# Optimization experiments

Measured on AMD Instinct MI355X. Metric: run time of the kernel, lower is better.

The kernel has to match this reference:

```python
import jax, jax.numpy as jnp
import numpy as np

B, T, C = 4, 2048, 1024
H = 16
HD = C // H  # 64


def setup_inputs() -> dict:
    key = jax.random.key(0)
    ks = jax.random.split(key, 4)
    x = jax.random.normal(ks[0], (B, T, C), dtype=jnp.float32)
    # c_attn: Linear(C, 3C, bias=False)  (qkv_bias=False)
    w_attn = jax.random.normal(ks[1], (C, 3 * C), dtype=jnp.float32) / np.sqrt(C)
    # c_proj: Linear(C, C) with bias (nn.Linear default)
    w_proj = jax.random.normal(ks[2], (C, C), dtype=jnp.float32) / np.sqrt(C)
    b_proj = jax.random.normal(ks[3], (C,), dtype=jnp.float32) * 0.01
    return {"x": x, "w_attn": w_attn, "w_proj": w_proj, "b_proj": b_proj}


def reference(x, w_attn, w_proj, b_proj):
    b, t, c = x.shape
    qkv = x @ w_attn  # [B,T,3C]
    q, k, v = jnp.split(qkv, 3, axis=-1)
    # [B,H,T,HD]
    q = q.reshape(b, t, H, HD).transpose(0, 2, 1, 3)
    k = k.reshape(b, t, H, HD).transpose(0, 2, 1, 3)
    v = v.reshape(b, t, H, HD).transpose(0, 2, 1, 3)
    scale = 1.0 / np.sqrt(HD)
    attn = jnp.einsum('bhqd,bhkd->bhqk', q, k) * scale  # [B,H,T,T]
    causal = jnp.tril(jnp.ones((t, t), dtype=bool))
    attn = jnp.where(causal, attn, -jnp.inf)
    attn = jax.nn.softmax(attn, axis=-1)
    out = jnp.einsum('bhqk,bhkd->bhqd', attn, v)  # [B,H,T,HD]
    out = out.transpose(0, 2, 1, 3).reshape(b, t, c)
    return out @ w_proj + b_proj
```

## Files before the change

### kernel.cpp

```cpp
#include <hip/hip_runtime.h>

#define BB 4
#define TT 2048
#define CC 1024
#define C3 3072
#define HH 16
#define HD 64
#define BT 8192

#define TS 32
#define TSZ (64 * TS)

typedef __bf16 bf16x8 __attribute__((ext_vector_type(8)));
typedef float floatx4 __attribute__((ext_vector_type(4)));
typedef unsigned uintx2 __attribute__((ext_vector_type(2)));
typedef unsigned short u16;

__device__ __forceinline__ u16 f2bf(float f) {
  union { float f; unsigned u; } a; a.f = f;
  return (u16)((a.u + 0x7fffu + ((a.u >> 16) & 1u)) >> 16);
}
__device__ __forceinline__ bf16x8 ld8(const u16* p) { return *(const bf16x8*)p; }
__device__ __forceinline__ floatx4 mfma16(bf16x8 a, bf16x8 b, floatx4 c) {
  return __builtin_amdgcn_mfma_f32_16x16x32_bf16(a, b, c, 0, 0, 0);
}

__device__ __forceinline__ void qd_xchg(unsigned a, unsigned b,
                                        unsigned& r0, unsigned& r1) {
  uintx2 t = __builtin_amdgcn_permlane32_swap(a, b, false, false);
  uintx2 r = __builtin_amdgcn_permlane16_swap(t[0], t[1], false, false);
  r0 = r[0]; r1 = r[1];
}

__global__ __launch_bounds__(256) void tobf16_kernel(const float4* __restrict__ src,
                                                     ushort4* __restrict__ dst, int n4) {
  int i = blockIdx.x * 256 + threadIdx.x;
  if (i >= n4) return;
  float4 v = src[i];
  ushort4 o; o.x = f2bf(v.x); o.y = f2bf(v.y); o.z = f2bf(v.z); o.w = f2bf(v.w);
  dst[i] = o;
}

__global__ __launch_bounds__(256) void transpose_bf16_kernel(const float* __restrict__ src,
                                                             u16* __restrict__ dst,
                                                             int K, int N) {
  __shared__ float s[64][65];
  const int t = threadIdx.x;
  const int r = t >> 4;
  const int c = (t & 15) * 4;
  const int k0 = blockIdx.y * 64, n0 = blockIdx.x * 64;
#pragma unroll
  for (int i = 0; i < 4; ++i) {
    float4 v = *(const float4*)&src[(size_t)(k0 + r + i * 16) * N + n0 + c];
    s[r + i * 16][c + 0] = v.x; s[r + i * 16][c + 1] = v.y;
    s[r + i * 16][c + 2] = v.z; s[r + i * 16][c + 3] = v.w;
  }
  __syncthreads();
#pragma unroll
  for (int i = 0; i < 4; ++i) {
    const int nn = r + i * 16;
    ushort4 o;
    o.x = f2bf(s[c + 0][nn]); o.y = f2bf(s[c + 1][nn]);
    o.z = f2bf(s[c + 2][nn]); o.w = f2bf(s[c + 3][nn]);
    *(ushort4*)&dst[(size_t)(n0 + nn) * K + k0 + c] = o;
  }
}

template<int MODE>
__global__ __launch_bounds__(256) void gemm_kernel(
    const u16* __restrict__ A, const u16* __restrict__ B,
    const float* __restrict__ bias, float* __restrict__ outf,
    u16* __restrict__ qk, u16* __restrict__ vT,
    int M, int N, int K) {
  __shared__ u16 smem[2][2][2 * TSZ];

  const int t = threadIdx.x;
  const int w = t >> 6, lane = t & 63, lr = lane & 15, qd = lane >> 4;
  const int wm = w >> 1, wn = w & 1;
  const int m0 = blockIdx.y * 128, n0 = blockIdx.x * 128;

  const int sr = t >> 2;
  const int sc = (t & 3) * 8;
  const int so = sr * TS + sc;
  const u16* Ag = A + (size_t)(m0 + sr) * K + sc;
  const u16* Bg = B + (size_t)(n0 + sr) * K + sc;

  floatx4 acc[4][4] = {};

  uint4 rA0, rA1, rB0, rB1;
  rA0 = *(const uint4*)(Ag);
  rA1 = *(const uint4*)(Ag + (size_t)64 * K);
  rB0 = *(const uint4*)(Bg);
  rB1 = *(const uint4*)(Bg + (size_t)64 * K);

  for (int k0 = 0; k0 < K; k0 += 32) {
    const int p = (k0 >> 5) & 1;
    u16* sA = &smem[p][0][0];
    u16* sB = &smem[p][1][0];
    *(uint4*)&sA[so]       = rA0;
    *(uint4*)&sA[TSZ + so] = rA1;
    *(uint4*)&sB[so]       = rB0;
    *(uint4*)&sB[TSZ + so] = rB1;
    __syncthreads();
    if (k0 + 32 < K) {
      rA0 = *(const uint4*)(Ag + k0 + 32);
      rA1 = *(const uint4*)(Ag + (size_t)64 * K + k0 + 32);
      rB0 = *(const uint4*)(Bg + k0 + 32);
      rB1 = *(const uint4*)(Bg + (size_t)64 * K + k0 + 32);
    }

    bf16x8 af[4], bf[4];
#pragma unroll
    for (int mj = 0; mj < 4; ++mj) af[mj] = ld8(&sA[(wm * 64 + mj * 16 + lr) * TS + qd * 8]);
#pragma unroll
    for (int nj = 0; nj < 4; ++nj) bf[nj] = ld8(&sB[(wn * 64 + nj * 16 + lr) * TS + qd * 8]);
#pragma unroll
    for (int mj = 0; mj < 4; ++mj)
#pragma unroll
      for (int nj = 0; nj < 4; ++nj)
        acc[mj][nj] = mfma16(af[mj], bf[nj], acc[mj][nj]);
  }

  const int rowg0 = m0 + wm * 64;
  const int colg0 = n0 + wn * 64;
  if constexpr (MODE == 2) {
#pragma unroll
    for (int nj = 0; nj < 4; ++nj) {
      const int col = colg0 + nj * 16 + lr;
      const float bv = bias[col];
#pragma unroll
      for (int mj = 0; mj < 4; ++mj)
#pragma unroll
        for (int i = 0; i < 4; ++i)
          outf[(size_t)(rowg0 + mj * 16 + qd * 4 + i) * N + col] = acc[mj][nj][i] + bv;
    }
  } else {
    __syncthreads();
    u16* Tw = &smem[0][0][0] + w * (32 * 72);
    const bool isV = (n0 >= 2 * CC);
    if (!isV) {
      const float qs = (n0 < CC) ? 0.18033688011f : 1.0f;
#pragma unroll
      for (int half = 0; half < 2; ++half) {
#pragma unroll
        for (int m2 = 0; m2 < 2; ++m2)
#pragma unroll
          for (int nj = 0; nj < 4; ++nj)
#pragma unroll
            for (int i = 0; i < 4; ++i)
              Tw[(m2 * 16 + qd * 4 + i) * 72 + nj * 16 + lr] =
                  f2bf(acc[half * 2 + m2][nj][i] * qs);
#pragma unroll
        for (int s = 0; s < 4; ++s) {
          const int rl = s * 8 + (lane >> 3);
          const int c0 = (lane & 7) * 8;
          *(bf16x8*)&qk[(size_t)(rowg0 + half * 32 + rl) * (2 * CC) + colg0 + c0] =
              ld8(&Tw[rl * 72 + c0]);
        }
      }
    } else {
      const int bI = m0 >> 11;
      const int tbase = (m0 & (TT - 1)) + wm * 64;
      const int dim0 = colg0 - 2 * CC;
#pragma unroll
      for (int half = 0; half < 2; ++half) {
#pragma unroll
        for (int n2 = 0; n2 < 2; ++n2)
#pragma unroll
          for (int mj = 0; mj < 4; ++mj)
#pragma unroll
            for (int i = 0; i < 4; ++i)
              Tw[(n2 * 16 + lr) * 72 + mj * 16 + qd * 4 + i] =
                  f2bf(acc[mj][half * 2 + n2][i]);
#pragma unroll
        for (int s = 0; s < 4; ++s) {
          const int dl = s * 8 + (lane >> 3);
          const int t0 = (lane & 7) * 8;
          *(bf16x8*)&vT[((size_t)(bI << 10) + dim0 + half * 32 + dl) * TT + tbase + t0] =
              ld8(&Tw[dl * 72 + t0]);
        }
      }
    }
  }
}

__global__ __launch_bounds__(256, 5) void attn_kernel(const u16* __restrict__ qk,
                                                      const u16* __restrict__ vT,
                                                      u16* __restrict__ att) {
  __shared__ u16 sKV[2][4][TSZ];

  const int t = threadIdx.x;
  const int w = t >> 6, lane = t & 63, lr = lane & 15, qd = lane >> 4;
  const int qtile = 31 - blockIdx.y;
  const int bh = blockIdx.x;
  const int b = bh >> 4, h = bh & 15;
  const int q0 = qtile * 64;
  const u16* qbase = qk + (size_t)b * TT * (2 * CC);

  const u16* qp = qbase + (size_t)(q0 + w * 16 + lr) * (2 * CC) + h * HD;
  const bf16x8 qf0 = ld8(qp + qd * 8);
  const bf16x8 qf1 = ld8(qp + 32 + qd * 8);

  const int sr = t >> 2, sc = (t & 3) * 8;
  const int so = sr * TS + sc;
  const u16* Kg = qbase + (size_t)sr * (2 * CC) + CC + h * HD + sc;
  const u16* Vg = vT + ((size_t)bh * HD + sr) * TT + sc;

  float lsum = 0.f;
  floatx4 o[4] = {};
  const int myq = q0 + w * 16 + lr;

  uint4 rK0, rK1, rV0, rV1;
  rK0 = *(const uint4*)(Kg);
  rK1 = *(const uint4*)(Kg + 32);
  rV0 = *(const uint4*)(Vg);
  rV1 = *(const uint4*)(Vg + 32);

  for (int kt = 0; kt <= qtile; ++kt) {
    u16* base = &sKV[kt & 1][0][0];
    *(uint4*)&base[so]           = rK0;
    *(uint4*)&base[TSZ + so]     = rK1;
    *(uint4*)&base[2 * TSZ + so] = rV0;
    *(uint4*)&base[3 * TSZ + so] = rV1;
    __syncthreads();
    if (kt < qtile) {
      const int kn = (kt + 1) * 64;
      rK0 = *(const uint4*)(Kg + (size_t)kn * (2 * CC));
      rK1 = *(const uint4*)(Kg + (size_t)kn * (2 * CC) + 32);
      rV0 = *(const uint4*)(Vg + kn);
      rV1 = *(const uint4*)(Vg + kn + 32);
    }

    const u16* sK0 = &sKV[kt & 1][0][0];
    const u16* sK1 = &sKV[kt & 1][1][0];
    const u16* sV0 = &sKV[kt & 1][2][0];
    const u16* sV1 = &sKV[kt & 1][3][0];

    floatx4 s[4] = {};
#pragma unroll
    for (int j = 0; j < 4; ++j) {
      bf16x8 kf0 = ld8(&sK0[(j * 16 + lr) * TS + qd * 8]);
      bf16x8 kf1 = ld8(&sK1[(j * 16 + lr) * TS + qd * 8]);
      s[j] = mfma16(kf0, qf0, s[j]);
      s[j] = mfma16(kf1, qf1, s[j]);
    }

    const bool diag = (kt == qtile);
    unsigned W[4][2];
#pragma unroll
    for (int j = 0; j < 4; ++j) {
      float p[4];
#pragma unroll
      for (int i = 0; i < 4; ++i) {
        p[i] = __builtin_amdgcn_exp2f(s[j][i]);
        if (diag) {
          const int key = kt * 64 + j * 16 + qd * 4 + i;
          p[i] = (key <= myq) ? p[i] : 0.f;
        }
        lsum += p[i];
      }
      W[j][0] = __builtin_amdgcn_perm(__float_as_uint(p[1]), __float_as_uint(p[0]), 0x07060302);
      W[j][1] = __builtin_amdgcn_perm(__float_as_uint(p[3]), __float_as_uint(p[2]), 0x07060302);
    }

    uint4 F0, F1;
    qd_xchg(W[0][0], W[1][0], F0.x, F0.z);
    qd_xchg(W[0][1], W[1][1], F0.y, F0.w);
    qd_xchg(W[2][0], W[3][0], F1.x, F1.z);
    qd_xchg(W[2][1], W[3][1], F1.y, F1.w);
    const bf16x8 pf0 = __builtin_bit_cast(bf16x8, F0);
    const bf16x8 pf1 = __builtin_bit_cast(bf16x8, F1);

#pragma unroll
    for (int j = 0; j < 4; ++j) {
      bf16x8 vf0 = ld8(&sV0[(j * 16 + lr) * TS + qd * 8]);
      bf16x8 vf1 = ld8(&sV1[(j * 16 + lr) * TS + qd * 8]);
      o[j] = mfma16(pf0, vf0, o[j]);
      o[j] = mfma16(pf1, vf1, o[j]);
    }
  }

  lsum += __shfl_xor(lsum, 16);
  lsum += __shfl_xor(lsum, 32);
  float linv[4];
#pragma unroll
  for (int i = 0; i < 4; ++i) linv[i] = 1.0f / __shfl(lsum, qd * 4 + i);

#pragma unroll
  for (int j = 0; j < 4; ++j)
#pragma unroll
    for (int i = 0; i < 4; ++i) {
      const size_t row = (size_t)b * TT + q0 + w * 16 + qd * 4 + i;
      att[row * CC + h * HD + j * 16 + lr] = f2bf(o[j][i] * linv[i]);
    }
}

extern "C" void kernel_launch(void* const* d_in, const int* in_sizes, int n_in,
                              void* d_out, int out_size, void* d_ws, size_t ws_size,
                              hipStream_t stream) {
  const float* x      = (const float*)d_in[0];
  const float* w_attn = (const float*)d_in[1];
  const float* w_proj = (const float*)d_in[2];
  const float* b_proj = (const float*)d_in[3];
  float* out = (float*)d_out;

  char* ws = (char*)d_ws;
  u16* xb  = (u16*)(ws + 0);
  u16* waT = (u16*)(ws + 16777216);
  u16* wpT = (u16*)(ws + 23068672);
  u16* qk  = (u16*)(ws + 25165824);
  u16* vT  = (u16*)(ws + 58720256);
  u16* att = (u16*)(ws + 75497472);

  tobf16_kernel<<<8192, 256, 0, stream>>>((const float4*)x, (ushort4*)xb, 2097152);
  transpose_bf16_kernel<<<dim3(48, 16), 256, 0, stream>>>(w_attn, waT, CC, C3);
  transpose_bf16_kernel<<<dim3(16, 16), 256, 0, stream>>>(w_proj, wpT, CC, CC);

  gemm_kernel<1><<<dim3(24, 64), 256, 0, stream>>>(xb, waT, nullptr, nullptr, qk, vT,
                                                   BT, C3, CC);
  attn_kernel<<<dim3(64, 32), 256, 0, stream>>>(qk, vT, att);

  gemm_kernel<2><<<dim3(8, 64), 256, 0, stream>>>(att, wpT, b_proj, out, nullptr, nullptr,
                                                  BT, CC, CC);
}
```

Before: 243.1 us.

## Stage GEMM and attention tiles via direct global-to-LDS loads

Replaces the register-staged global loads followed by LDS stores with global_load_lds builtins that write 16 bytes per lane straight into shared memory, in both the GEMM and attention kernels. The double-buffer schedule changes so the next tile is loaded into the other buffer before compute, with a barrier at the end of each iteration. This saves VGPRs and the separate ds_write instructions. It relies on the per-wave contiguous LDS placement (wave base plus lane*16 bytes) matching the old row/column layout, and on the barrier waiting for the asynchronous LDS writes to finish.

```diff
diff --git a/kernel.cpp b/kernel.cpp
--- a/kernel.cpp
+++ b/kernel.cpp
@@ -23,6 +23,12 @@
 __device__ __forceinline__ bf16x8 ld8(const u16* p) { return *(const bf16x8*)p; }
 __device__ __forceinline__ floatx4 mfma16(bf16x8 a, bf16x8 b, floatx4 c) {
   return __builtin_amdgcn_mfma_f32_16x16x32_bf16(a, b, c, 0, 0, 0);
+}
+
+__device__ __forceinline__ void gload16(const u16* g, u16* l) {
+  __builtin_amdgcn_global_load_lds(
+      (const __attribute__((address_space(1))) void*)g,
+      (__attribute__((address_space(3))) void*)l, 16, 0, 0);
 }
 
 __device__ __forceinline__ void qd_xchg(unsigned a, unsigned b,
@@ -81,33 +87,34 @@
 
   const int sr = t >> 2;
   const int sc = (t & 3) * 8;
-  const int so = sr * TS + sc;
+  const int wb = (t & ~63) * 8;
   const u16* Ag = A + (size_t)(m0 + sr) * K + sc;
   const u16* Bg = B + (size_t)(n0 + sr) * K + sc;
 
   floatx4 acc[4][4] = {};
 
-  uint4 rA0, rA1, rB0, rB1;
-  rA0 = *(const uint4*)(Ag);
-  rA1 = *(const uint4*)(Ag + (size_t)64 * K);
-  rB0 = *(const uint4*)(Bg);
-  rB1 = *(const uint4*)(Bg + (size_t)64 * K);
+  {
+    u16* sA = &smem[0][0][0];
+    u16* sB = &smem[0][1][0];
+    gload16(Ag,                  &sA[wb]);
+    gload16(Ag + (size_t)64 * K, &sA[TSZ + wb]);
+    gload16(Bg,                  &sB[wb]);
+    gload16(Bg + (size_t)64 * K, &sB[TSZ + wb]);
+  }
+  __syncthreads();
 
   for (int k0 = 0; k0 < K; k0 += 32) {
     const int p = (k0 >> 5) & 1;
-    u16* sA = &smem[p][0][0];
-    u16* sB = &smem[p][1][0];
-    *(uint4*)&sA[so]       = rA0;
-    *(uint4*)&sA[TSZ + so] = rA1;
-    *(uint4*)&sB[so]       = rB0;
-    *(uint4*)&sB[TSZ + so] = rB1;
-    __syncthreads();
     if (k0 + 32 < K) {
-      rA0 = *(const uint4*)(Ag + k0 + 32);
-      rA1 = *(const uint4*)(Ag + (size_t)64 * K + k0 + 32);
-      rB0 = *(const uint4*)(Bg + k0 + 32);
-      rB1 = *(const uint4*)(Bg + (size_t)64 * K + k0 + 32);
-    }
+      u16* sA = &smem[p ^ 1][0][0];
+      u16* sB = &smem[p ^ 1][1][0];
+      gload16(Ag + k0 + 32,                  &sA[wb]);
+      gload16(Ag + (size_t)64 * K + k0 + 32, &sA[TSZ + wb]);
+      gload16(Bg + k0 + 32,                  &sB[wb]);
+      gload16(Bg + (size_t)64 * K + k0 + 32, &sB[TSZ + wb]);
+    }
+    const u16* sA = &smem[p][0][0];
+    const u16* sB = &smem[p][1][0];
 
     bf16x8 af[4], bf[4];
 #pragma unroll
@@ -119,6 +126,7 @@
 #pragma unroll
       for (int nj = 0; nj < 4; ++nj)
         acc[mj][nj] = mfma16(af[mj], bf[nj], acc[mj][nj]);
+    __syncthreads();
   }
 
   const int rowg0 = m0 + wm * 64;
@@ -135,7 +143,6 @@
           outf[(size_t)(rowg0 + mj * 16 + qd * 4 + i) * N + col] = acc[mj][nj][i] + bv;
     }
   } else {
-    __syncthreads();
     u16* Tw = &smem[0][0][0] + w * (32 * 72);
     const bool isV = (n0 >= 2 * CC);
     if (!isV) {
@@ -202,7 +209,7 @@
   const bf16x8 qf1 = ld8(qp + 32 + qd * 8);
 
   const int sr = t >> 2, sc = (t & 3) * 8;
-  const int so = sr * TS + sc;
+  const int wb = (t & ~63) * 8;
   const u16* Kg = qbase + (size_t)sr * (2 * CC) + CC + h * HD + sc;
   const u16* Vg = vT + ((size_t)bh * HD + sr) * TT + sc;
 
@@ -210,25 +217,23 @@
   floatx4 o[4] = {};
   const int myq = q0 + w * 16 + lr;
 
-  uint4 rK0, rK1, rV0, rV1;
-  rK0 = *(const uint4*)(Kg);
-  rK1 = *(const uint4*)(Kg + 32);
-  rV0 = *(const uint4*)(Vg);
-  rV1 = *(const uint4*)(Vg + 32);
+  {
+    u16* b0 = &sKV[0][0][0];
+    gload16(Kg,      &b0[wb]);
+    gload16(Kg + 32, &b0[TSZ + wb]);
+    gload16(Vg,      &b0[2 * TSZ + wb]);
+    gload16(Vg + 32, &b0[3 * TSZ + wb]);
+  }
+  __syncthreads();
 
   for (int kt = 0; kt <= qtile; ++kt) {
-    u16* base = &sKV[kt & 1][0][0];
-    *(uint4*)&base[so]           = rK0;
-    *(uint4*)&base[TSZ + so]     = rK1;
-    *(uint4*)&base[2 * TSZ + so] = rV0;
-    *(uint4*)&base[3 * TSZ + so] = rV1;
-    __syncthreads();
     if (kt < qtile) {
       const int kn = (kt + 1) * 64;
-      rK0 = *(const uint4*)(Kg + (size_t)kn * (2 * CC));
-      rK1 = *(const uint4*)(Kg + (size_t)kn * (2 * CC) + 32);
-      rV0 = *(const uint4*)(Vg + kn);
-      rV1 = *(const uint4*)(Vg + kn + 32);
+      u16* bn = &sKV[(kt + 1) & 1][0][0];
+      gload16(Kg + (size_t)kn * (2 * CC),      &bn[wb]);
+      gload16(Kg + (size_t)kn * (2 * CC) + 32, &bn[TSZ + wb]);
+      gload16(Vg + kn,                         &bn[2 * TSZ + wb]);
+      gload16(Vg + kn + 32,                    &bn[3 * TSZ + wb]);
     }
 
     const u16* sK0 = &sKV[kt & 1][0][0];
@@ -278,6 +283,7 @@
       o[j] = mfma16(pf0, vf0, o[j]);
       o[j] = mfma16(pf1, vf1, o[j]);
     }
+    __syncthreads();
   }
 
   lsum += __shfl_xor(lsum, 16);
```

New measurement: 236.2 us. 1.03x faster.
